# Kernel optimization log

Hardware: AMD Instinct MI355X
Metric: run time of the kernel (lower is better)

Reference implementation:

```python
import jax, jax.numpy as jnp
import numpy as np

N_NODES = 10000
N_EDGES = 640000
F_IN = 128
F_HID = 128
BN_EPS = 1e-5


def _spectral_norm_weight(W, u):
    # One power iteration, matching torch.nn.utils.spectral_norm defaults.
    v = W.T @ u
    v = v / (jnp.linalg.norm(v) + 1e-12)
    u_new = W @ v
    u_new = u_new / (jnp.linalg.norm(u_new) + 1e-12)
    sigma = u_new @ (W @ v)
    return W / sigma


def setup_inputs() -> dict:
    key = jax.random.key(0)
    ks = jax.random.split(key, 8)
    x = jax.random.normal(ks[0], (N_NODES, F_IN), dtype=jnp.float32)
    edge_index = jax.random.randint(ks[1], (2, N_EDGES), 0, N_NODES, dtype=jnp.int64)
    W1 = jax.random.normal(ks[2], (F_HID, F_IN), dtype=jnp.float32) * (1.0 / np.sqrt(F_IN))
    b1 = jax.random.normal(ks[3], (F_HID,), dtype=jnp.float32) * 0.01
    u1 = jax.random.normal(ks[4], (F_HID,), dtype=jnp.float32)
    gamma = jnp.ones((F_HID,), dtype=jnp.float32)
    beta = jnp.zeros((F_HID,), dtype=jnp.float32)
    W2 = jax.random.normal(ks[5], (F_HID, F_HID), dtype=jnp.float32) * (1.0 / np.sqrt(F_HID))
    b2 = jax.random.normal(ks[6], (F_HID,), dtype=jnp.float32) * 0.01
    u2 = jax.random.normal(ks[7], (F_HID,), dtype=jnp.float32)
    return {"x": x, "edge_index": edge_index, "W1": W1, "b1": b1, "u1": u1,
            "gamma": gamma, "beta": beta, "W2": W2, "b2": b2, "u2": u2}


def reference(x, edge_index, W1, b1, u1, gamma, beta, W2, b2, u2):
    src, dst = edge_index[0], edge_index[1]
    # GINConv sum aggregation: out_i = sum_{j in N(i)} x_j
    agg = jax.ops.segment_sum(x[src], dst, num_segments=N_NODES)
    h = x + agg  # eps = 0 (default, train_eps=False)
    # MLP: SN-Linear -> ReLU -> BatchNorm1d (training stats) -> SN-Linear
    h = h @ _spectral_norm_weight(W1, u1).T + b1
    h = jax.nn.relu(h)
    mu = jnp.mean(h, axis=0)
    var = jnp.mean((h - mu) ** 2, axis=0)  # biased var, as torch BN forward
    h = gamma * (h - mu) / jnp.sqrt(var + BN_EPS) + beta
    h = h @ _spectral_norm_weight(W2, u2).T + b2
    return h
```

## Files before the change

### kernel.cpp

```cpp
#include <hip/hip_runtime.h>

#define NF 128
#define FB 128
#define CB 64
#define MAXNODE 10240

__device__ __forceinline__ unsigned short f2bf(float f) {
    unsigned int u = __float_as_uint(f);
    unsigned int r = u + 0x7FFFu + ((u >> 16) & 1u);
    return (unsigned short)(r >> 16);
}

__global__ __launch_bounds__(512) void power_hist_kernel(
    const float* __restrict__ W1, const float* __restrict__ u1,
    const float* __restrict__ W2, const float* __restrict__ u2,
    const int* __restrict__ dst, int n_edges,
    int* __restrict__ hist2d, int nbin,
    const float* __restrict__ x, unsigned short* __restrict__ xb, int n_x4,
    float* __restrict__ inv_sigma, float* __restrict__ W1t,
    float* __restrict__ colzero, int* __restrict__ cnts) {
    __shared__ float Wl[128][129];
    __shared__ float us[128], vv[128], part[4][128], red[128];
    __shared__ int hist[MAXNODE];
    int tid = threadIdx.x;

    if (blockIdx.x >= 2 + FB) {
        int cb = blockIdx.x - 2 - FB;
        const float4* x4 = (const float4*)x;
        ushort4* xb4 = (ushort4*)xb;
        for (int i = cb * 512 + tid; i < n_x4; i += CB * 512) {
            float4 v = x4[i];
            ushort4 o;
            o.x = f2bf(v.x); o.y = f2bf(v.y); o.z = f2bf(v.z); o.w = f2bf(v.w);
            xb4[i] = o;
        }
        return;
    }
    if (blockIdx.x >= 2) {
        int fb = blockIdx.x - 2;
        for (int i = tid; i < nbin; i += 512) hist[i] = 0;
        __syncthreads();
        int chunk = (n_edges + FB - 1) / FB;
        int e0 = fb * chunk, e1 = min(e0 + chunk, n_edges);
        int a0 = min(e1, (e0 + 3) & ~3);
        for (int e = e0 + tid; e < a0; e += 512) atomicAdd(&hist[dst[e]], 1);
        const int4* d4 = (const int4*)dst;
        int vs = a0 >> 2, ve = e1 >> 2;
        for (int i = vs + tid; i < ve; i += 512) {
            int4 d = d4[i];
            atomicAdd(&hist[d.x], 1);
            atomicAdd(&hist[d.y], 1);
            atomicAdd(&hist[d.z], 1);
            atomicAdd(&hist[d.w], 1);
        }
        for (int e = (ve << 2) + tid; e < e1; e += 512)
            if (e >= a0) atomicAdd(&hist[dst[e]], 1);
        __syncthreads();
        for (int i = tid; i < nbin; i += 512) hist2d[(size_t)fb * nbin + i] = hist[i];
        return;
    }

    const float* W = blockIdx.x ? W2 : W1;
    const float* u = blockIdx.x ? u2 : u1;
    const float4* W4 = (const float4*)W;
    for (int j = tid; j < 4096; j += 512) {
        float4 w = W4[j];
        int r = j >> 5, c0 = (j & 31) << 2;
        Wl[r][c0] = w.x; Wl[r][c0 + 1] = w.y; Wl[r][c0 + 2] = w.z; Wl[r][c0 + 3] = w.w;
    }
    if (tid < 128) us[tid] = u[tid];
    if (blockIdx.x == 0 && tid >= 256 && tid < 512) colzero[tid - 256] = 0.f;
    if (blockIdx.x == 0 && tid < 2) cnts[tid] = 0;
    __syncthreads();

    int c = tid & 127, sl = tid >> 7;
    float acc = 0.f;
#pragma unroll
    for (int j = 0; j < 32; ++j) acc = fmaf(Wl[sl * 32 + j][c], us[sl * 32 + j], acc);
    part[sl][c] = acc;
    __syncthreads();
    if (tid < 128) {
        float v = part[0][tid] + part[1][tid] + part[2][tid] + part[3][tid];
        vv[tid] = v;
        red[tid] = v * v;
    }
    __syncthreads();
    for (int s = 64; s > 0; s >>= 1) { if (tid < s) red[tid] += red[tid + s]; __syncthreads(); }
    float nv = sqrtf(red[0]) + 1e-12f;
    __syncthreads();
    if (tid < 128) vv[tid] = vv[tid] / nv;
    __syncthreads();

    float t = 0.f;
#pragma unroll
    for (int k = 0; k < 32; ++k) t = fmaf(Wl[c][sl * 32 + k], vv[sl * 32 + k], t);
    part[sl][c] = t;
    __syncthreads();
    if (tid < 128) {
        float tv = part[0][tid] + part[1][tid] + part[2][tid] + part[3][tid];
        red[tid] = tv * tv;
    }
    __syncthreads();
    for (int s = 64; s > 0; s >>= 1) { if (tid < s) red[tid] += red[tid + s]; __syncthreads(); }
    float tt = red[0];
    float is = (sqrtf(tt) + 1e-12f) / tt;
    if (tid == 0) inv_sigma[blockIdx.x] = is;
    if (blockIdx.x == 0) {
        for (int idx = tid; idx < 16384; idx += 512) {
            int k = idx >> 7, j = idx & 127;
            W1t[idx] = Wl[j][k] * is;
        }
    }
}

__global__ __launch_bounds__(1024) void scanAB_kernel(int* __restrict__ hist2d,
                                                      int* __restrict__ binOff,
                                                      int nbin, int* __restrict__ cnt) {
    int tid = threadIdx.x;
    int bin = blockIdx.x * 1024 + tid;
    if (bin < nbin) {
        int run = 0;
#pragma unroll 4
        for (int fb = 0; fb < FB; ++fb) {
            int v = hist2d[(size_t)fb * nbin + bin];
            hist2d[(size_t)fb * nbin + bin] = run;
            run += v;
        }
        binOff[bin] = run;
    }
    __threadfence();
    __syncthreads();
    __shared__ int isLast;
    if (tid == 0) isLast = (atomicAdd(cnt, 1) == (int)gridDim.x - 1);
    __syncthreads();
    if (!isLast) return;
    __threadfence();

    __shared__ int wsum[16], wexcl[16];
    __shared__ int carry_s;
    int lane = tid & 63, wv = tid >> 6;
    if (tid == 0) carry_s = 0;
    __syncthreads();
    int nr = (nbin + 1023) >> 10;
    for (int r = 0; r < nr; ++r) {
        int i = (r << 10) + tid;
        int v = (i < nbin) ? binOff[i] : 0;
        int inc = v;
        for (int off = 1; off < 64; off <<= 1) {
            int t = __shfl_up(inc, off);
            if (lane >= off) inc += t;
        }
        if (lane == 63) wsum[wv] = inc;
        __syncthreads();
        if (wv == 0) {
            int s = (lane < 16) ? wsum[lane] : 0;
            int si = s;
            for (int off = 1; off < 16; off <<= 1) {
                int t = __shfl_up(si, off);
                if (lane >= off) si += t;
            }
            if (lane < 16) wexcl[lane] = si - s;
        }
        __syncthreads();
        int excl = inc - v + wexcl[wv] + carry_s;
        if (i < nbin) binOff[i] = excl;
        __syncthreads();
        if (tid == 1023) carry_s += wexcl[15] + wsum[15];
        __syncthreads();
    }
    if (tid == 0) binOff[nbin] = carry_s;
}

__global__ __launch_bounds__(512) void fill_kernel(
    const int* __restrict__ src, const int* __restrict__ dst,
    const int* __restrict__ hist2d, const int* __restrict__ binOff,
    int* __restrict__ bucket, int nbin, int n_edges) {
    __shared__ int cur[MAXNODE];
    int tid = threadIdx.x, fb = blockIdx.x;
    for (int i = tid; i < nbin; i += 512)
        cur[i] = hist2d[(size_t)fb * nbin + i] + binOff[i];
    __syncthreads();
    int chunk = (n_edges + FB - 1) / FB;
    int e0 = fb * chunk, e1 = min(e0 + chunk, n_edges);
    int a0 = min(e1, (e0 + 3) & ~3);
    for (int e = e0 + tid; e < a0; e += 512) {
        int pos = atomicAdd(&cur[dst[e]], 1);
        bucket[pos] = src[e];
    }
    const int4* d4 = (const int4*)dst;
    const int4* s4 = (const int4*)src;
    int vs = a0 >> 2, ve = e1 >> 2;
    for (int i = vs + tid; i < ve; i += 512) {
        int4 d = d4[i];
        int4 s = s4[i];
        int p0 = atomicAdd(&cur[d.x], 1);
        int p1 = atomicAdd(&cur[d.y], 1);
        int p2 = atomicAdd(&cur[d.z], 1);
        int p3 = atomicAdd(&cur[d.w], 1);
        bucket[p0] = s.x; bucket[p1] = s.y; bucket[p2] = s.z; bucket[p3] = s.w;
    }
    for (int e = (ve << 2) + tid; e < e1; e += 512)
        if (e >= a0) {
            int pos = atomicAdd(&cur[dst[e]], 1);
            bucket[pos] = src[e];
        }
}

__global__ __launch_bounds__(256) void gather_kernel(
    const unsigned short* __restrict__ xb, const int* __restrict__ bucket,
    const int* __restrict__ binOff, float* __restrict__ h0, int n_nodes) {
    int gw = (blockIdx.x * blockDim.x + threadIdx.x) >> 6;
    int lane = threadIdx.x & 63;
    if (gw >= n_nodes) return;
    const unsigned int* xu = (const unsigned int*)xb;
    unsigned int u0 = xu[(size_t)gw * 64 + lane];
    float2 acc;
    acc.x = __uint_as_float(u0 << 16);
    acc.y = __uint_as_float(u0 & 0xFFFF0000u);
    int j = binOff[gw], end = binOff[gw + 1];
    for (; j + 8 <= end; j += 8) {
        int s0 = bucket[j],     s1 = bucket[j + 1], s2 = bucket[j + 2], s3 = bucket[j + 3];
        int s4 = bucket[j + 4], s5 = bucket[j + 5], s6 = bucket[j + 6], s7 = bucket[j + 7];
        unsigned int v0 = xu[(size_t)s0 * 64 + lane];
        unsigned int v1 = xu[(size_t)s1 * 64 + lane];
        unsigned int v2 = xu[(size_t)s2 * 64 + lane];
        unsigned int v3 = xu[(size_t)s3 * 64 + lane];
        unsigned int v4 = xu[(size_t)s4 * 64 + lane];
        unsigned int v5 = xu[(size_t)s5 * 64 + lane];
        unsigned int v6 = xu[(size_t)s6 * 64 + lane];
        unsigned int v7 = xu[(size_t)s7 * 64 + lane];
        acc.x += __uint_as_float(v0 << 16) + __uint_as_float(v1 << 16)
               + __uint_as_float(v2 << 16) + __uint_as_float(v3 << 16)
               + __uint_as_float(v4 << 16) + __uint_as_float(v5 << 16)
               + __uint_as_float(v6 << 16) + __uint_as_float(v7 << 16);
        acc.y += __uint_as_float(v0 & 0xFFFF0000u) + __uint_as_float(v1 & 0xFFFF0000u)
               + __uint_as_float(v2 & 0xFFFF0000u) + __uint_as_float(v3 & 0xFFFF0000u)
               + __uint_as_float(v4 & 0xFFFF0000u) + __uint_as_float(v5 & 0xFFFF0000u)
               + __uint_as_float(v6 & 0xFFFF0000u) + __uint_as_float(v7 & 0xFFFF0000u);
    }
    for (; j < end; ++j) {
        unsigned int v = xu[(size_t)bucket[j] * 64 + lane];
        acc.x += __uint_as_float(v << 16);
        acc.y += __uint_as_float(v & 0xFFFF0000u);
    }
    ((float2*)h0)[(size_t)gw * 64 + lane] = acc;
}

__global__ void edge_scatter_kernel(const int* __restrict__ ei, const float* __restrict__ x,
                                    float* __restrict__ h0, int n_edges) {
    int gtid = blockIdx.x * blockDim.x + threadIdx.x;
    int wid = gtid >> 6;
    int lane = threadIdx.x & 63;
    int nw = (gridDim.x * blockDim.x) >> 6;
    const int* srcs = ei;
    const int* dsts = ei + n_edges;
    for (int e = wid; e < n_edges; e += nw) {
        int s = srcs[e];
        int d = dsts[e];
        atomicAdd(&h0[d * NF + lane], x[s * NF + lane]);
        atomicAdd(&h0[d * NF + 64 + lane], x[s * NF + 64 + lane]);
    }
}

template <bool RELU, bool BNACC>
__global__ __launch_bounds__(256, 4) void gemm16_kernel(
    const float* __restrict__ H, const float* __restrict__ Wt,
    const float* __restrict__ bias, float* __restrict__ O,
    float* __restrict__ colsum, float* __restrict__ colsumsq, int n_rows) {
    __shared__ float Hl[16][128];
    int tid = threadIdx.x;
    int m0 = blockIdx.x * 16;

    const float4* H4 = (const float4*)H;
    for (int j = tid; j < 512; j += 256) {
        int r = j >> 5, k4 = j & 31;
        int gr = m0 + r;
        float4 h = (gr < n_rows) ? H4[(size_t)gr * 32 + k4] : make_float4(0.f, 0.f, 0.f, 0.f);
        *(float4*)&Hl[r][k4 << 2] = h;
    }
    __syncthreads();

    int tx = tid & 31, ty = tid >> 5;
    int rb = ty * 2, cb = tx * 4;
    float acc[2][4] = {};
    const float4* Wt4 = (const float4*)Wt;

#pragma unroll 2
    for (int k = 0; k < 128; k += 4) {
        float4 w0 = Wt4[(k + 0) * 32 + tx];
        float4 w1 = Wt4[(k + 1) * 32 + tx];
        float4 w2 = Wt4[(k + 2) * 32 + tx];
        float4 w3 = Wt4[(k + 3) * 32 + tx];
        float wv[4][4] = {{w0.x, w0.y, w0.z, w0.w}, {w1.x, w1.y, w1.z, w1.w},
                          {w2.x, w2.y, w2.z, w2.w}, {w3.x, w3.y, w3.z, w3.w}};
#pragma unroll
        for (int i = 0; i < 2; ++i) {
            float4 h = *(const float4*)&Hl[rb + i][k];
            float hf[4] = {h.x, h.y, h.z, h.w};
#pragma unroll
            for (int kk = 0; kk < 4; ++kk)
#pragma unroll
                for (int j = 0; j < 4; ++j)
                    acc[i][j] = fmaf(hf[kk], wv[kk][j], acc[i][j]);
        }
    }

    float bv[4];
#pragma unroll
    for (int j = 0; j < 4; ++j) bv[j] = bias[cb + j];

    float s[4] = {0.f, 0.f, 0.f, 0.f}, q[4] = {0.f, 0.f, 0.f, 0.f};
#pragma unroll
    for (int i = 0; i < 2; ++i) {
        int gr = m0 + rb + i;
        if (gr < n_rows) {
            float o[4];
#pragma unroll
            for (int j = 0; j < 4; ++j) {
                float v = acc[i][j] + bv[j];
                if (RELU) v = fmaxf(v, 0.f);
                o[j] = v;
                if (BNACC) { s[j] += v; q[j] = fmaf(v, v, q[j]); }
            }
            *(float4*)&O[(size_t)gr * NF + cb] = make_float4(o[0], o[1], o[2], o[3]);
        }
    }

    if (BNACC) {
        __syncthreads();
        float* sS = &Hl[0][0];
        float* sQ = &Hl[8][0];
#pragma unroll
        for (int j = 0; j < 4; ++j) {
            sS[ty * 128 + cb + j] = s[j];
            sQ[ty * 128 + cb + j] = q[j];
        }
        __syncthreads();
        if (tid < 128) {
            float ts = 0.f, tq = 0.f;
#pragma unroll
            for (int g = 0; g < 8; ++g) {
                ts += sS[g * 128 + tid];
                tq += sQ[g * 128 + tid];
            }
            atomicAdd(&colsum[tid], ts);
            atomicAdd(&colsumsq[tid], tq);
        }
    }
}

__global__ void fold_kernel(const float* __restrict__ W2, const float* __restrict__ b2,
                            const float* __restrict__ gamma, const float* __restrict__ beta,
                            const float* __restrict__ colsum, const float* __restrict__ colsumsq,
                            const float* __restrict__ inv_sigma, float* __restrict__ W2pt,
                            float* __restrict__ b2p, float inv_n) {
    __shared__ float a[128], cc[128], red[128];
    int k = threadIdx.x;
    int j = blockIdx.x;
    float mu = colsum[k] * inv_n;
    float var = colsumsq[k] * inv_n - mu * mu;
    float ai = gamma[k] / sqrtf(var + 1e-5f);
    a[k] = ai;
    cc[k] = beta[k] - ai * mu;
    __syncthreads();
    float is2 = inv_sigma[1];
    float wv = W2[j * 128 + k] * is2;
    W2pt[k * 128 + j] = wv * a[k];
    red[k] = wv * cc[k];
    __syncthreads();
    for (int s = 64; s > 0; s >>= 1) { if (k < s) red[k] += red[k + s]; __syncthreads(); }
    if (k == 0) b2p[j] = b2[j] + red[0];
}

extern "C" void kernel_launch(void* const* d_in, const int* in_sizes, int n_in,
                              void* d_out, int out_size, void* d_ws, size_t ws_size,
                              hipStream_t stream) {
    const float* x     = (const float*)d_in[0];
    const int*   ei    = (const int*)d_in[1];
    const float* W1    = (const float*)d_in[2];
    const float* b1    = (const float*)d_in[3];
    const float* u1    = (const float*)d_in[4];
    const float* gamma = (const float*)d_in[5];
    const float* beta  = (const float*)d_in[6];
    const float* W2    = (const float*)d_in[7];
    const float* b2    = (const float*)d_in[8];
    const float* u2    = (const float*)d_in[9];
    float* out = (float*)d_out;

    int n_nodes = in_sizes[0] / NF;
    int n_edges = in_sizes[1] / 2;
    int nbin = n_nodes;
    int nbin_pad = (nbin + 1 + 3) & ~3;
    int nedge_pad = (n_edges + 3) & ~3;
    size_t scratch = (size_t)FB * nbin > (size_t)n_nodes * NF
                   ? (size_t)FB * nbin : (size_t)n_nodes * NF;
    scratch = (scratch + 3) & ~(size_t)3;

    float* ws        = (float*)d_ws;
    float* inv_sigma = ws;
    float* colsum    = ws + 4;
    float* colsumsq  = colsum + 128;
    float* W1t       = colsumsq + 128;
    float* W2pt      = W1t + 16384;
    float* b2p       = W2pt + 16384;
    int*   cnts      = (int*)(b2p + 128);
    int*   binOff    = cnts + 4;
    int*   bucket    = binOff + nbin_pad;
    int*   hist2d    = bucket + nedge_pad;
    float* h0        = (float*)hist2d;
    unsigned short* xb = (unsigned short*)(hist2d + scratch);
    float* h0g       = (float*)(xb + (size_t)n_nodes * NF);

    size_t need = (size_t)(33160 + nbin_pad + nedge_pad + scratch) * 4
                + (size_t)n_nodes * NF * 2 + (size_t)n_nodes * NF * 4;
    bool fused = (n_nodes <= MAXNODE) && (ws_size >= need);

    int n_x4 = n_nodes * 32;
    int gemm_blocks = (n_nodes + 15) / 16;

    if (fused) {
        power_hist_kernel<<<2 + FB + CB, 512, 0, stream>>>(
            W1, u1, W2, u2, ei + n_edges, n_edges, hist2d, nbin,
            x, xb, n_x4, inv_sigma, W1t, colsum, cnts);
        scanAB_kernel<<<(nbin + 1023) / 1024, 1024, 0, stream>>>(hist2d, binOff, nbin,
                                                                 &cnts[0]);
        fill_kernel<<<FB, 512, 0, stream>>>(ei, ei + n_edges, hist2d, binOff, bucket,
                                            nbin, n_edges);
        gather_kernel<<<(n_nodes * 64 + 255) / 256, 256, 0, stream>>>(
            xb, bucket, binOff, h0g, n_nodes);
        gemm16_kernel<true, true><<<gemm_blocks, 256, 0, stream>>>(
            h0g, W1t, b1, out, colsum, colsumsq, n_nodes);
    } else {
        power_hist_kernel<<<2, 512, 0, stream>>>(
            W1, u1, W2, u2, ei + n_edges, n_edges, hist2d, nbin,
            x, xb, 0, inv_sigma, W1t, colsum, cnts);
        hipMemcpyAsync(h0, x, (size_t)n_nodes * NF * sizeof(float),
                       hipMemcpyDeviceToDevice, stream);
        edge_scatter_kernel<<<2048, 256, 0, stream>>>(ei, x, h0, n_edges);
        gemm16_kernel<true, true><<<gemm_blocks, 256, 0, stream>>>(
            h0, W1t, b1, out, colsum, colsumsq, n_nodes);
    }

    fold_kernel<<<128, 128, 0, stream>>>(W2, b2, gamma, beta, colsum, colsumsq,
                                         inv_sigma, W2pt, b2p, 1.0f / (float)n_nodes);

    gemm16_kernel<false, false><<<gemm_blocks, 256, 0, stream>>>(
        out, W2pt, b2p, out, nullptr, nullptr, n_nodes);
}
```

Measured before the change: 133.8 us.

## Parallelize per-bin histogram scan across feature blocks via shared-memory tiles

The column scan over the 128 fill-block histograms is restructured. Each block now handles 64 bins and stages a 128x64 tile in shared memory, then splits the serial 128-step prefix into 8 segments of 16 with a partial-sum combine. Before, each thread walked all 128 rows serially, and there were only about 10 blocks. The change raises the block count and the parallelism of the scan. In exchange it adds shared-memory traffic and extra barriers, and the final single-block scan over bins now takes twice as many rounds.

```diff
diff --git a/kernel.cpp b/kernel.cpp
--- a/kernel.cpp
+++ b/kernel.cpp
@@ -3,6 +3,7 @@
 #define NF 128
 #define FB 128
 #define CB 64
+#define BPB 64
 #define MAXNODE 10240
 
 __device__ __forceinline__ unsigned short f2bf(float f) {
@@ -113,21 +114,48 @@
     }
 }
 
-__global__ __launch_bounds__(1024) void scanAB_kernel(int* __restrict__ hist2d,
-                                                      int* __restrict__ binOff,
-                                                      int nbin, int* __restrict__ cnt) {
+__global__ __launch_bounds__(512) void scanAB_kernel(int* __restrict__ hist2d,
+                                                     int* __restrict__ binOff,
+                                                     int nbin, int* __restrict__ cnt) {
+    __shared__ int tile[128][BPB + 1];
+    __shared__ int part[8][BPB];
     int tid = threadIdx.x;
-    int bin = blockIdx.x * 1024 + tid;
-    if (bin < nbin) {
-        int run = 0;
-#pragma unroll 4
-        for (int fb = 0; fb < FB; ++fb) {
-            int v = hist2d[(size_t)fb * nbin + bin];
-            hist2d[(size_t)fb * nbin + bin] = run;
-            run += v;
-        }
-        binOff[bin] = run;
-    }
+    int bin0 = blockIdx.x * BPB;
+
+    for (int i = tid; i < 128 * BPB; i += 512) {
+        int fb = i >> 6, b = i & (BPB - 1);
+        int bin = bin0 + b;
+        tile[fb][b] = (bin < nbin) ? hist2d[(size_t)fb * nbin + bin] : 0;
+    }
+    __syncthreads();
+
+    int g = tid >> 3, s = tid & 7;
+    int fb0 = s << 4;
+    int partial = 0;
+#pragma unroll
+    for (int f = 0; f < 16; ++f) partial += tile[fb0 + f][g];
+    part[s][g] = partial;
+    __syncthreads();
+    int excl = 0;
+#pragma unroll
+    for (int t = 0; t < 8; ++t)
+        if (t < s) excl += part[t][g];
+    int run = excl;
+#pragma unroll
+    for (int f = 0; f < 16; ++f) {
+        int v = tile[fb0 + f][g];
+        tile[fb0 + f][g] = run;
+        run += v;
+    }
+    if (s == 7 && bin0 + g < nbin) binOff[bin0 + g] = run;
+    __syncthreads();
+
+    for (int i = tid; i < 128 * BPB; i += 512) {
+        int fb = i >> 6, b = i & (BPB - 1);
+        int bin = bin0 + b;
+        if (bin < nbin) hist2d[(size_t)fb * nbin + bin] = tile[fb][b];
+    }
+
     __threadfence();
     __syncthreads();
     __shared__ int isLast;
@@ -136,14 +164,14 @@
     if (!isLast) return;
     __threadfence();
 
-    __shared__ int wsum[16], wexcl[16];
+    __shared__ int wsum[8], wexcl[8];
     __shared__ int carry_s;
     int lane = tid & 63, wv = tid >> 6;
     if (tid == 0) carry_s = 0;
     __syncthreads();
-    int nr = (nbin + 1023) >> 10;
+    int nr = (nbin + 511) >> 9;
     for (int r = 0; r < nr; ++r) {
-        int i = (r << 10) + tid;
+        int i = (r << 9) + tid;
         int v = (i < nbin) ? binOff[i] : 0;
         int inc = v;
         for (int off = 1; off < 64; off <<= 1) {
@@ -152,20 +180,17 @@
         }
         if (lane == 63) wsum[wv] = inc;
         __syncthreads();
-        if (wv == 0) {
-            int s = (lane < 16) ? wsum[lane] : 0;
-            int si = s;
-            for (int off = 1; off < 16; off <<= 1) {
-                int t = __shfl_up(si, off);
-                if (lane >= off) si += t;
-            }
-            if (lane < 16) wexcl[lane] = si - s;
-        }
-        __syncthreads();
-        int excl = inc - v + wexcl[wv] + carry_s;
-        if (i < nbin) binOff[i] = excl;
-        __syncthreads();
-        if (tid == 1023) carry_s += wexcl[15] + wsum[15];
+        if (wv == 0 && lane < 8) {
+            int si = 0;
+            for (int t = 0; t < 8; ++t)
+                if (t < lane) si += wsum[t];
+            wexcl[lane] = si;
+        }
+        __syncthreads();
+        int ex = inc - v + wexcl[wv] + carry_s;
+        if (i < nbin) binOff[i] = ex;
+        __syncthreads();
+        if (tid == 511) carry_s += wexcl[7] + wsum[7];
         __syncthreads();
     }
     if (tid == 0) binOff[nbin] = carry_s;
@@ -422,8 +447,8 @@
         power_hist_kernel<<<2 + FB + CB, 512, 0, stream>>>(
             W1, u1, W2, u2, ei + n_edges, n_edges, hist2d, nbin,
             x, xb, n_x4, inv_sigma, W1t, colsum, cnts);
-        scanAB_kernel<<<(nbin + 1023) / 1024, 1024, 0, stream>>>(hist2d, binOff, nbin,
-                                                                 &cnts[0]);
+        scanAB_kernel<<<(nbin + BPB - 1) / BPB, 512, 0, stream>>>(hist2d, binOff, nbin,
+                                                                  &cnts[0]);
         fill_kernel<<<FB, 512, 0, stream>>>(ei, ei + n_edges, hist2d, binOff, bucket,
                                             nbin, n_edges);
         gather_kernel<<<(n_nodes * 64 + 255) / 256, 256, 0, stream>>>(
```

Measured after the change: 143.0 us. +6.8%, slower.
